# Performance work log

Measured on AMD Instinct MI355X. Metric: run time of the kernel, lower is better.

## Reference

```python
import jax, jax.numpy as jnp
import numpy as np

N_NODES = 50000
N_EDGES = 800000
D = 64
N_TYPES = 4


def setup_inputs() -> dict:
    key = jax.random.key(0)
    ks = jax.random.split(key, 7)
    x = jax.random.normal(ks[0], (N_NODES, D), dtype=jnp.float32)
    vec = jax.random.normal(ks[1], (N_NODES, 3, D), dtype=jnp.float32)
    node_type = jax.random.randint(ks[2], (N_NODES,), 0, N_TYPES)
    src = jax.random.randint(ks[3], (N_EDGES,), 0, N_NODES)
    dst = jax.random.randint(ks[4], (N_EDGES,), 0, N_NODES)
    # per-node-type conv weights (one scalar-channel and one vector-channel matrix per type)
    W_s = jax.random.normal(ks[5], (N_TYPES, D, D), dtype=jnp.float32) / np.sqrt(D)
    W_v = jax.random.normal(ks[6], (N_TYPES, D, D), dtype=jnp.float32) / np.sqrt(D)
    return {"x": x, "vec\u0065c"[0:3]: vec, "node_type": node_type, "src": src, "dst": dst, "W_s": W_s, "W_v": W_v}


def reference(x, vec, node_type, src, dst, W_s, W_v):
    """HeteroVertexConv: for each node type t, take the in-subgraph (edges whose
    destination is of type t), run a linear message-passing conv, and accumulate
    the result at type-t destination nodes only.
    Returns (srsts, vrsts) = new (data.x, data.vec)."""
    n_nodes = x.shape[0]
    n_types = W_s.shape[0]
    srsts = jnp.zeros_like(x)          # [N, D]
    vrsts = jnp.zeros_like(vec)        # [N, 3, D]
    dst_type = node_type[dst]          # [E] type of each edge's destination
    for t in range(n_types):           # small fixed loop over node types
        emask = (dst_type == t)
        # type-t projection of all node features (equiv. to conv on the in-subgraph)
        proj_s = x @ W_s[t]                                   # [N, D]
        proj_v = jnp.einsum('ncd,de->nce', vec, W_v[t])       # [N, 3, D]
        # per-edge messages, zeroed for edges whose dst is not type t
        msg_s = jnp.where(emask[:, None], proj_s[src], 0.0)           # [E, D]
        msg_v = jnp.where(emask[:, None, None], proj_v[src], 0.0)    # [E, 3, D]
        # scatter-add into destinations; only type-t nodes receive mass
        srsts = srsts + jax.ops.segment_sum(msg_s, dst, num_segments=n_nodes)
        vrsts = vrsts + jax.ops.segment_sum(msg_v, dst, num_segments=n_nodes)
    return srsts, vrsts
```

## Files before the change

### kernel.cpp

```cpp
#include <hip/hip_runtime.h>

#define D 64
#define CAP 64
#define PBK 256
#define EPB 2048


typedef float f32x4 __attribute__((ext_vector_type(4)));

__device__ __forceinline__ unsigned bf16rne(float f) {
    unsigned u = __float_as_uint(f);
    return (u + 0x7fffu + ((u >> 16) & 1u)) >> 16;
}
__device__ __forceinline__ float bf_lo(unsigned w) { return __uint_as_float(w << 16); }
__device__ __forceinline__ float bf_hi(unsigned w) { return __uint_as_float(w & 0xffff0000u); }

__device__ __forceinline__ void acc8(float (&a)[8], const uint4& v) {
    a[0] += bf_lo(v.x); a[1] += bf_hi(v.x);
    a[2] += bf_lo(v.y); a[3] += bf_hi(v.y);
    a[4] += bf_lo(v.z); a[5] += bf_hi(v.z);
    a[6] += bf_lo(v.w); a[7] += bf_hi(v.w);
}

__global__ __launch_bounds__(256) void k_pack_part(
    const float* __restrict__ x, const float* __restrict__ vec,
    const int* __restrict__ src, const int* __restrict__ dst,
    uint4* __restrict__ packed,
    int* __restrict__ gcur,
    unsigned* __restrict__ bucket,
    int n_edges, int n_nodes, int rng, int ecap, int eb1)
{
    if ((int)blockIdx.x >= eb1) {
        int idx = ((int)blockIdx.x - eb1) * 256 + threadIdx.x;
        if (idx >= n_nodes * 32) return;
        int n = idx >> 5, j = idx & 31;
        int ei = j * 8;
        const float* sp = (ei < 64) ? (x + (size_t)n * 64 + ei)
                                    : (vec + (size_t)n * 192 + (ei - 64));
        f32x4 f0 = __builtin_nontemporal_load((const f32x4*)sp);
        f32x4 f1 = __builtin_nontemporal_load((const f32x4*)(sp + 4));
        uint4 w;
        w.x = bf16rne(f0.x) | (bf16rne(f0.y) << 16);
        w.y = bf16rne(f0.z) | (bf16rne(f0.w) << 16);
        w.z = bf16rne(f1.x) | (bf16rne(f1.y) << 16);
        w.w = bf16rne(f1.z) | (bf16rne(f1.w) << 16);
        packed[idx] = w;
        return;
    }

    __shared__ int h[PBK];
    __shared__ int lcur[PBK];
    int tid = threadIdx.x;
    for (int i = tid; i < PBK; i += 256) h[i] = 0;
    __syncthreads();

    int e0 = (int)blockIdx.x * EPB;
    int d[8], s[8], b[8];
#pragma unroll
    for (int r = 0; r < 8; ++r) {
        int e = e0 + r * 256 + tid;
        bool v = (e < n_edges);
        d[r] = v ? __builtin_nontemporal_load(dst + e) : 0;
        s[r] = v ? __builtin_nontemporal_load(src + e) : 0;
        b[r] = v ? (d[r] / rng) : -1;
        if (v) atomicAdd(&h[b[r]], 1);
    }
    __syncthreads();
    if (tid < PBK) {
        int c = h[tid];
        lcur[tid] = (c > 0) ? atomicAdd(&gcur[tid * 16], c) : 0;
    }
    __syncthreads();
#pragma unroll
    for (int r = 0; r < 8; ++r) {
        if (b[r] >= 0) {
            int pos = atomicAdd(&lcur[b[r]], 1);
            if (pos < ecap)
                bucket[(size_t)b[r] * ecap + pos] =
                    ((unsigned)d[r] << 16) | (unsigned)s[r];
        }
    }
}

__global__ __launch_bounds__(256) void k_slots(
    const unsigned* __restrict__ bucket, const int* __restrict__ gcur,
    int* __restrict__ slots, int* __restrict__ counts,
    int n_nodes, int rng, int ecap)
{
    __shared__ int lc[256];
    int b = blockIdx.x;
    int n0 = b * rng;
    int nend = n0 + rng; if (nend > n_nodes) nend = n_nodes;
    int nloc = nend - n0;
    if (nloc <= 0) return;
    for (int i = threadIdx.x; i < nloc; i += 256) lc[i] = 0;
    __syncthreads();
    int cnt = gcur[b * 16]; if (cnt > ecap) cnt = ecap;
    const unsigned* bp = bucket + (size_t)b * ecap;
    for (int i = threadIdx.x; i < cnt; i += 256) {
        unsigned rec = bp[i];
        int dd = (int)(rec >> 16);
        int ss = (int)(rec & 0xFFFFu);
        int slot = atomicAdd(&lc[dd - n0], 1);
        if (slot < CAP) slots[(size_t)dd * CAP + slot] = ss;
    }
    __syncthreads();
    for (int i = threadIdx.x; i < nloc; i += 256) counts[n0 + i] = lc[i];
}

__global__ __launch_bounds__(256) void k_gather_project(
    const uint4* __restrict__ packed, const int* __restrict__ node_type,
    const float* __restrict__ W_s, const float* __restrict__ W_v,
    const int* __restrict__ counts, const int* __restrict__ slots,
    float* __restrict__ out_s, float* __restrict__ out_v, int n_nodes)
{
    int wave = threadIdx.x >> 6;
    int lane = threadIdx.x & 63;
    int n = blockIdx.x * 4 + wave;
    if (n >= n_nodes) return;
    int half = lane >> 5, hl = lane & 31;

    int t = node_type[n];
    int cnt = counts[n]; if (cnt > CAP) cnt = CAP;
    int myidx = __builtin_nontemporal_load(slots + (size_t)n * CAP + lane);

    float a[8];
#pragma unroll
    for (int i = 0; i < 8; ++i) a[i] = 0.f;

    int k = 0;
    for (; k + 16 <= cnt; k += 16) {
        int s[8]; uint4 w[8];
#pragma unroll
        for (int u = 0; u < 8; ++u) s[u] = __shfl(myidx, k + 2 * u + half);
#pragma unroll
        for (int u = 0; u < 8; ++u) w[u] = packed[(size_t)s[u] * 32 + hl];
#pragma unroll
        for (int u = 0; u < 8; ++u) acc8(a, w[u]);
    }
    for (; k + 8 <= cnt; k += 8) {
        int s0 = __shfl(myidx, k     + half);
        int s1 = __shfl(myidx, k + 2 + half);
        int s2 = __shfl(myidx, k + 4 + half);
        int s3 = __shfl(myidx, k + 6 + half);
        uint4 w0 = packed[(size_t)s0 * 32 + hl];
        uint4 w1 = packed[(size_t)s1 * 32 + hl];
        uint4 w2 = packed[(size_t)s2 * 32 + hl];
        uint4 w3 = packed[(size_t)s3 * 32 + hl];
        acc8(a, w0); acc8(a, w1); acc8(a, w2); acc8(a, w3);
    }
    for (; k + 2 <= cnt; k += 2) {
        int s = __shfl(myidx, k + half);
        uint4 w = packed[(size_t)s * 32 + hl];
        acc8(a, w);
    }
    if (k < cnt) {
        int s = __shfl(myidx, k);
        if (half == 0) { uint4 w = packed[(size_t)s * 32 + hl]; acc8(a, w); }
    }
#pragma unroll
    for (int i = 0; i < 8; ++i) a[i] += __shfl_xor(a[i], 32);

    const float* Ws = W_s + (size_t)t * D * D;
    const float* Wv = W_v + (size_t)t * D * D;
    float ys = 0.f, y0 = 0.f, y1 = 0.f, y2 = 0.f;
#pragma unroll
    for (int g = 0; g < 8; ++g) {
        float ws[8], wv[8];
#pragma unroll
        for (int u = 0; u < 8; ++u) {
            ws[u] = Ws[(g * 8 + u) * D + lane];
            wv[u] = Wv[(g * 8 + u) * D + lane];
        }
#pragma unroll
        for (int u = 0; u < 8; ++u) {
            float as  = __shfl(a[u],      g);
            float av0 = __shfl(a[u],  8 + g);
            float av1 = __shfl(a[u], 16 + g);
            float av2 = __shfl(a[u], 24 + g);
            ys = fmaf(as,  ws[u], ys);
            y0 = fmaf(av0, wv[u], y0);
            y1 = fmaf(av1, wv[u], y1);
            y2 = fmaf(av2, wv[u], y2);
        }
    }
    __builtin_nontemporal_store(ys, &out_s[(size_t)n * D + lane]);
    float* ov = out_v + (size_t)n * 3 * D;
    __builtin_nontemporal_store(y0, &ov[lane]);
    __builtin_nontemporal_store(y1, &ov[D + lane]);
    __builtin_nontemporal_store(y2, &ov[2 * D + lane]);
}

__global__ __launch_bounds__(256) void k_hist(
    const int* __restrict__ dst, int* __restrict__ counts,
    int* __restrict__ pos, int n_edges)
{
    int e = blockIdx.x * 256 + threadIdx.x;
    if (e < n_edges) pos[e] = atomicAdd(&counts[dst[e]], 1);
}
__global__ __launch_bounds__(256) void k_base(
    const int* __restrict__ counts, int* __restrict__ base,
    int* __restrict__ cursor, int n_nodes)
{
    int n = blockIdx.x * 256 + threadIdx.x;
    if (n < n_nodes) base[n] = atomicAdd(cursor, counts[n]);
}
__global__ __launch_bounds__(256) void k_fill(
    const int* __restrict__ src, const int* __restrict__ dst,
    const int* __restrict__ base, const int* __restrict__ pos,
    int* __restrict__ csr, int n_edges)
{
    int e = blockIdx.x * 256 + threadIdx.x;
    if (e < n_edges) csr[base[dst[e]] + pos[e]] = src[e];
}
__global__ __launch_bounds__(256) void k_gather_project_f32(
    const float* __restrict__ x, const float* __restrict__ vec,
    const int* __restrict__ node_type,
    const float* __restrict__ W_s, const float* __restrict__ W_v,
    const int* __restrict__ counts, const int* __restrict__ base,
    const int* __restrict__ csr,
    float* __restrict__ out_s, float* __restrict__ out_v, int n_nodes)
{
    __shared__ float agg[4][4 * D];
    int wave = threadIdx.x >> 6, lane = threadIdx.x & 63;
    int ch = lane >> 4, q = lane & 15;
    int n = blockIdx.x * 4 + wave;
    int cnt = 0, b = 0, t = 0;
    if (n < n_nodes) { cnt = counts[n]; b = base[n]; t = node_type[n]; }
    bool isx = (ch == 0);
    const float4* bp = isx ? (const float4*)x : (const float4*)vec;
    int stride4 = isx ? 16 : 48;
    int off4 = isx ? q : (ch - 1) * 16 + q;
    float4 acc = make_float4(0.f, 0.f, 0.f, 0.f);
    for (int k = 0; k < cnt; ++k) {
        int s = csr[b + k];
        float4 r = bp[(size_t)s * stride4 + off4];
        acc.x += r.x; acc.y += r.y; acc.z += r.z; acc.w += r.w;
    }
    *(float4*)&agg[wave][ch * D + q * 4] = acc;
    __syncthreads();
    if (n >= n_nodes) return;
    const float* Ws = W_s + (size_t)t * D * D;
    const float* Wv = W_v + (size_t)t * D * D;
    const float* a0 = &agg[wave][0];
    float ys = 0.f, y0 = 0.f, y1 = 0.f, y2 = 0.f;
#pragma unroll 8
    for (int i = 0; i < D; ++i) {
        float wsi = Ws[i * D + lane], wvi = Wv[i * D + lane];
        ys = fmaf(a0[i], wsi, ys);
        y0 = fmaf(a0[D + i], wvi, y0);
        y1 = fmaf(a0[2 * D + i], wvi, y1);
        y2 = fmaf(a0[3 * D + i], wvi, y2);
    }
    out_s[(size_t)n * D + lane] = ys;
    float* ov = out_v + (size_t)n * 3 * D;
    ov[lane] = y0; ov[D + lane] = y1; ov[2 * D + lane] = y2;
}

extern "C" void kernel_launch(void* const* d_in, const int* in_sizes, int n_in,
                              void* d_out, int out_size, void* d_ws, size_t ws_size,
                              hipStream_t stream) {
    const float* x         = (const float*)d_in[0];
    const float* vec       = (const float*)d_in[1];
    const int*   node_type = (const int*)d_in[2];
    const int*   src       = (const int*)d_in[3];
    const int*   dst       = (const int*)d_in[4];
    const float* W_s       = (const float*)d_in[5];
    const float* W_v       = (const float*)d_in[6];

    int n_nodes = in_sizes[2];
    int n_edges = in_sizes[3];

    float* out_s = (float*)d_out;
    float* out_v = out_s + (size_t)n_nodes * D;

    int eb = (n_edges + 255) / 256;

    int rng  = (n_nodes + PBK - 1) / PBK;
    int ecap = (n_edges + PBK - 1) / PBK * 2 + 256;
    size_t packed_bytes = (size_t)n_nodes * 32 * sizeof(uint4);
    size_t slots_bytes  = (size_t)n_nodes * CAP * sizeof(int);
    size_t counts_bytes = (size_t)n_nodes * sizeof(int);
    size_t gcur_bytes   = (size_t)PBK * 16 * sizeof(int);
    size_t bucket_bytes = (size_t)PBK * ecap * sizeof(unsigned);
    size_t need_fast = packed_bytes + slots_bytes + counts_bytes
                     + gcur_bytes + bucket_bytes;

    if (ws_size >= need_fast && n_nodes <= 65536 && rng <= 256) {
        uint4*    packed = (uint4*)d_ws;
        int*      slots  = (int*)((char*)d_ws + packed_bytes);
        int*      counts = (int*)((char*)d_ws + packed_bytes + slots_bytes);
        int*      gcur   = (int*)((char*)d_ws + packed_bytes + slots_bytes + counts_bytes);
        unsigned* bucket = (unsigned*)((char*)d_ws + packed_bytes + slots_bytes
                                        + counts_bytes + gcur_bytes);

        (void)hipMemsetAsync(gcur, 0, gcur_bytes, stream);

        int eb1 = (n_edges + EPB - 1) / EPB;
        int pb  = (n_nodes * 32 + 255) / 256;
        k_pack_part<<<eb1 + pb, 256, 0, stream>>>(
            x, vec, src, dst, packed, gcur, bucket,
            n_edges, n_nodes, rng, ecap, eb1);

        k_slots<<<PBK, 256, 0, stream>>>(
            bucket, gcur, slots, counts, n_nodes, rng, ecap);

        int nb4 = (n_nodes + 3) / 4;
        k_gather_project<<<nb4, 256, 0, stream>>>(
            packed, node_type, W_s, W_v, counts, slots, out_s, out_v, n_nodes);
        return;
    }

    int* cursor = (int*)d_ws;
    int* counts = cursor + 1;
    int* base   = counts + n_nodes;
    int* pos    = base + n_nodes;
    int* csr    = pos + n_edges;
    int nb = (n_nodes + 255) / 256;
    int nb4 = (n_nodes + 3) / 4;
    (void)hipMemsetAsync(cursor, 0, (size_t)(1 + n_nodes) * sizeof(int), stream);
    k_hist<<<eb, 256, 0, stream>>>(dst, counts, pos, n_edges);
    k_base<<<nb, 256, 0, stream>>>(counts, base, cursor, n_nodes);
    k_fill<<<eb, 256, 0, stream>>>(src, dst, base, pos, csr, n_edges);
    k_gather_project_f32<<<nb4, 256, 0, stream>>>(
        x, vec, node_type, W_s, W_v, counts, base, csr, out_s, out_v, n_nodes);
}
```

Baseline: 275.8 us.

## Replace padded per-node slot table with compact 16-bit CSR built via shared-memory staging

The edge partition kernel now buckets edges by dst>>8 (fixed 256-node buckets) and stages them in shared memory sorted by bucket, so each bucket's global writes are contiguous. A new k_csr kernel prefix-sums the bucket counts and per-node counts and writes a compact uint16 CSR with per-node base offsets, replacing the padded N*64 int slot array. The gather kernel reads source indices from the compact CSR. This cuts scattered writes and the memory footprint of the index structure, at the cost of extra scans and syncs, a hard-coded bucket capacity (ECAP) and a node range limited to 16 bits.

Result: no change. 275.6 us (-0.1%).

```diff
diff --git a/kernel.cpp b/kernel.cpp
--- a/kernel.cpp
+++ b/kernel.cpp
@@ -2,8 +2,8 @@
 
 #define D 64
 #define CAP 64
-#define PBK 256
 #define EPB 2048
+#define ECAP 6144
 
 
 typedef float f32x4 __attribute__((ext_vector_type(4)));
@@ -28,7 +28,7 @@
     uint4* __restrict__ packed,
     int* __restrict__ gcur,
     unsigned* __restrict__ bucket,
-    int n_edges, int n_nodes, int rng, int ecap, int eb1)
+    int n_edges, int n_nodes, int eb1)
 {
     if ((int)blockIdx.x >= eb1) {
         int idx = ((int)blockIdx.x - eb1) * 256 + threadIdx.x;
@@ -48,10 +48,10 @@
         return;
     }
 
-    __shared__ int h[PBK];
-    __shared__ int lcur[PBK];
-    int tid = threadIdx.x;
-    for (int i = tid; i < PBK; i += 256) h[i] = 0;
+    __shared__ unsigned stage[EPB];
+    __shared__ int h[256], off[256], gbase[256], cur[256], wtot[4];
+    int tid = threadIdx.x, lane = tid & 63, wv = tid >> 6;
+    h[tid] = 0;
     __syncthreads();
 
     int e0 = (int)blockIdx.x * EPB;
@@ -62,56 +62,107 @@
         bool v = (e < n_edges);
         d[r] = v ? __builtin_nontemporal_load(dst + e) : 0;
         s[r] = v ? __builtin_nontemporal_load(src + e) : 0;
-        b[r] = v ? (d[r] / rng) : -1;
+        b[r] = v ? (d[r] >> 8) : -1;
         if (v) atomicAdd(&h[b[r]], 1);
     }
     __syncthreads();
-    if (tid < PBK) {
-        int c = h[tid];
-        lcur[tid] = (c > 0) ? atomicAdd(&gcur[tid * 16], c) : 0;
-    }
-    __syncthreads();
+
+    int hv = h[tid];
+    int inc = hv;
+#pragma unroll
+    for (int o = 1; o < 64; o <<= 1) { int tv = __shfl_up(inc, o); if (lane >= o) inc += tv; }
+    if (lane == 63) wtot[wv] = inc;
+    __syncthreads();
+    if (tid == 0) { int r = 0; for (int q = 0; q < 4; ++q) { int c = wtot[q]; wtot[q] = r; r += c; } }
+    __syncthreads();
+    int myoff = inc - hv + wtot[wv];
+    off[tid] = myoff;
+    cur[tid] = myoff;
+    gbase[tid] = (hv > 0) ? atomicAdd(&gcur[tid * 16], hv) : 0;
+    __syncthreads();
+
 #pragma unroll
     for (int r = 0; r < 8; ++r) {
         if (b[r] >= 0) {
-            int pos = atomicAdd(&lcur[b[r]], 1);
-            if (pos < ecap)
-                bucket[(size_t)b[r] * ecap + pos] =
-                    ((unsigned)d[r] << 16) | (unsigned)s[r];
+            int p = atomicAdd(&cur[b[r]], 1);
+            stage[p] = ((unsigned)d[r] << 16) | (unsigned)s[r];
         }
     }
-}
-
-__global__ __launch_bounds__(256) void k_slots(
+    __syncthreads();
+
+    int total = n_edges - e0; if (total > EPB) total = EPB;
+    for (int i = tid; i < total; i += 256) {
+        unsigned rec = stage[i];
+        int t = rec >> 24;
+        int dp = gbase[t] + (i - off[t]);
+        if (dp < ECAP) bucket[(size_t)t * ECAP + dp] = rec;
+    }
+}
+
+__global__ __launch_bounds__(256) void k_csr(
     const unsigned* __restrict__ bucket, const int* __restrict__ gcur,
-    int* __restrict__ slots, int* __restrict__ counts,
-    int n_nodes, int rng, int ecap)
-{
-    __shared__ int lc[256];
+    unsigned short* __restrict__ csr, int* __restrict__ counts,
+    int* __restrict__ baseo, int n_nodes, int nb)
+{
+    __shared__ unsigned short stg[ECAP];
+    __shared__ int pf[256], lc[256], wtot[4];
+    int tid = threadIdx.x, lane = tid & 63, wv = tid >> 6;
     int b = blockIdx.x;
-    int n0 = b * rng;
-    int nend = n0 + rng; if (nend > n_nodes) nend = n_nodes;
-    int nloc = nend - n0;
-    if (nloc <= 0) return;
-    for (int i = threadIdx.x; i < nloc; i += 256) lc[i] = 0;
-    __syncthreads();
-    int cnt = gcur[b * 16]; if (cnt > ecap) cnt = ecap;
-    const unsigned* bp = bucket + (size_t)b * ecap;
-    for (int i = threadIdx.x; i < cnt; i += 256) {
+
+    pf[tid] = (tid < nb) ? gcur[tid * 16] : 0;
+    lc[tid] = 0;
+    __syncthreads();
+
+    int pv = pf[tid];
+    int inc = pv;
+#pragma unroll
+    for (int o = 1; o < 64; o <<= 1) { int tv = __shfl_up(inc, o); if (lane >= o) inc += tv; }
+    if (lane == 63) wtot[wv] = inc;
+    __syncthreads();
+    if (tid == 0) { int r = 0; for (int q = 0; q < 4; ++q) { int c = wtot[q]; wtot[q] = r; r += c; } }
+    __syncthreads();
+    pf[tid] = inc - pv + wtot[wv];
+    __syncthreads();
+    int ebase = pf[b];
+    int cnt = gcur[b * 16]; if (cnt > ECAP) cnt = ECAP;
+    int n0 = b << 8;
+    int nloc = n_nodes - n0; if (nloc > 256) nloc = 256;
+    const unsigned* bp = bucket + (size_t)b * ECAP;
+
+    for (int i = tid; i < cnt; i += 256)
+        atomicAdd(&lc[(bp[i] >> 16) & 255], 1);
+    __syncthreads();
+
+    int cv = lc[tid];
+    int inc2 = cv;
+#pragma unroll
+    for (int o = 1; o < 64; o <<= 1) { int tv = __shfl_up(inc2, o); if (lane >= o) inc2 += tv; }
+    if (lane == 63) wtot[wv] = inc2;
+    __syncthreads();
+    if (tid == 0) { int r = 0; for (int q = 0; q < 4; ++q) { int c = wtot[q]; wtot[q] = r; r += c; } }
+    __syncthreads();
+    int nbv = inc2 - cv + wtot[wv];
+    if (tid < nloc) { counts[n0 + tid] = cv; baseo[n0 + tid] = ebase + nbv; }
+    __syncthreads();
+    lc[tid] = nbv;
+    __syncthreads();
+
+    for (int i = tid; i < cnt; i += 256) {
         unsigned rec = bp[i];
-        int dd = (int)(rec >> 16);
-        int ss = (int)(rec & 0xFFFFu);
-        int slot = atomicAdd(&lc[dd - n0], 1);
-        if (slot < CAP) slots[(size_t)dd * CAP + slot] = ss;
-    }
-    __syncthreads();
-    for (int i = threadIdx.x; i < nloc; i += 256) counts[n0 + i] = lc[i];
+        int p = atomicAdd(&lc[(rec >> 16) & 255], 1);
+        stg[p] = (unsigned short)(rec & 0xFFFFu);
+    }
+    __syncthreads();
+
+    for (int i = tid; i < cnt; i += 256)
+        csr[ebase + i] = stg[i];
 }
 
 __global__ __launch_bounds__(256) void k_gather_project(
     const uint4* __restrict__ packed, const int* __restrict__ node_type,
     const float* __restrict__ W_s, const float* __restrict__ W_v,
-    const int* __restrict__ counts, const int* __restrict__ slots,
+    const int* __restrict__ counts, const int* __restrict__ baseo,
+    const unsigned short* __restrict__ csr,
     float* __restrict__ out_s, float* __restrict__ out_v, int n_nodes)
 {
     int wave = threadIdx.x >> 6;
@@ -122,7 +173,8 @@
 
     int t = node_type[n];
     int cnt = counts[n]; if (cnt > CAP) cnt = CAP;
-    int myidx = __builtin_nontemporal_load(slots + (size_t)n * CAP + lane);
+    int base = baseo[n];
+    int myidx = (int)__builtin_nontemporal_load(csr + base + lane);
 
     float a[8];
 #pragma unroll
@@ -276,38 +328,40 @@
 
     int eb = (n_edges + 255) / 256;
 
-    int rng  = (n_nodes + PBK - 1) / PBK;
-    int ecap = (n_edges + PBK - 1) / PBK * 2 + 256;
+    int nb = (n_nodes + 255) >> 8;
     size_t packed_bytes = (size_t)n_nodes * 32 * sizeof(uint4);
-    size_t slots_bytes  = (size_t)n_nodes * CAP * sizeof(int);
+    size_t csr_bytes    = ((size_t)n_edges + 64) * sizeof(unsigned short);
+    csr_bytes = (csr_bytes + 15) & ~(size_t)15;
     size_t counts_bytes = (size_t)n_nodes * sizeof(int);
-    size_t gcur_bytes   = (size_t)PBK * 16 * sizeof(int);
-    size_t bucket_bytes = (size_t)PBK * ecap * sizeof(unsigned);
-    size_t need_fast = packed_bytes + slots_bytes + counts_bytes
-                     + gcur_bytes + bucket_bytes;
-
-    if (ws_size >= need_fast && n_nodes <= 65536 && rng <= 256) {
-        uint4*    packed = (uint4*)d_ws;
-        int*      slots  = (int*)((char*)d_ws + packed_bytes);
-        int*      counts = (int*)((char*)d_ws + packed_bytes + slots_bytes);
-        int*      gcur   = (int*)((char*)d_ws + packed_bytes + slots_bytes + counts_bytes);
-        unsigned* bucket = (unsigned*)((char*)d_ws + packed_bytes + slots_bytes
-                                        + counts_bytes + gcur_bytes);
+    size_t baseo_bytes  = (size_t)n_nodes * sizeof(int);
+    size_t gcur_bytes   = 256 * 16 * sizeof(int);
+    size_t bucket_bytes = (size_t)256 * ECAP * sizeof(unsigned);
+    size_t need_fast = packed_bytes + csr_bytes + counts_bytes
+                     + baseo_bytes + gcur_bytes + bucket_bytes;
+
+    if (ws_size >= need_fast && n_nodes <= 65536) {
+        char* p = (char*)d_ws;
+        uint4*          packed = (uint4*)p;             p += packed_bytes;
+        unsigned short* csr16  = (unsigned short*)p;    p += csr_bytes;
+        int*            counts = (int*)p;               p += counts_bytes;
+        int*            baseo  = (int*)p;               p += baseo_bytes;
+        int*            gcur   = (int*)p;               p += gcur_bytes;
+        unsigned*       bucket = (unsigned*)p;
 
         (void)hipMemsetAsync(gcur, 0, gcur_bytes, stream);
 
         int eb1 = (n_edges + EPB - 1) / EPB;
         int pb  = (n_nodes * 32 + 255) / 256;
         k_pack_part<<<eb1 + pb, 256, 0, stream>>>(
-            x, vec, src, dst, packed, gcur, bucket,
-            n_edges, n_nodes, rng, ecap, eb1);
-
-        k_slots<<<PBK, 256, 0, stream>>>(
-            bucket, gcur, slots, counts, n_nodes, rng, ecap);
+            x, vec, src, dst, packed, gcur, bucket, n_edges, n_nodes, eb1);
+
+        k_csr<<<nb, 256, 0, stream>>>(
+            bucket, gcur, csr16, counts, baseo, n_nodes, nb);
 
         int nb4 = (n_nodes + 3) / 4;
         k_gather_project<<<nb4, 256, 0, stream>>>(
-            packed, node_type, W_s, W_v, counts, slots, out_s, out_v, n_nodes);
+            packed, node_type, W_s, W_v, counts, baseo, csr16,
+            out_s, out_v, n_nodes);
         return;
     }
 
@@ -316,11 +370,11 @@
     int* base   = counts + n_nodes;
     int* pos    = base + n_nodes;
     int* csr    = pos + n_edges;
-    int nb = (n_nodes + 255) / 256;
+    int nbf = (n_nodes + 255) / 256;
     int nb4 = (n_nodes + 3) / 4;
     (void)hipMemsetAsync(cursor, 0, (size_t)(1 + n_nodes) * sizeof(int), stream);
     k_hist<<<eb, 256, 0, stream>>>(dst, counts, pos, n_edges);
-    k_base<<<nb, 256, 0, stream>>>(counts, base, cursor, n_nodes);
+    k_base<<<nbf, 256, 0, stream>>>(counts, base, cursor, n_nodes);
     k_fill<<<eb, 256, 0, stream>>>(src, dst, base, pos, csr, n_edges);
     k_gather_project_f32<<<nb4, 256, 0, stream>>>(
         x, vec, node_type, W_s, W_v, counts, base, csr, out_s, out_v, n_nodes);
```
